# Kernel optimization log

Measured on AMD Instinct MI355X. Metric: run time of the kernel, lower is better.

Reference implementation:

```python
import jax, jax.numpy as jnp
import numpy as np

N, E, K, D = 100000, 3200000, 1024, 11


def setup_inputs() -> dict:
    key = jax.random.key(0)
    ks = jax.random.split(key, 11)
    return {
        "x": jax.random.normal(ks[0], (N, D), jnp.float32),
        "edge_index": jax.random.randint(ks[1], (2, E), 0, N, dtype=jnp.int32),
        "ready_idx": jnp.sort(jax.random.randint(ks[2], (K,), 0, N, dtype=jnp.int32)),
        "W1": jax.random.normal(ks[3], (D, 64), jnp.float32) * 0.2,
        "b1": jax.random.normal(ks[4], (64,), jnp.float32) * 0.02,
        "W2": jax.random.normal(ks[5], (75, 1), jnp.float32) * 0.2,
        "b2": jax.random.normal(ks[6], (1,), jnp.float32) * 0.02,
        "Wd": jax.random.normal(ks[7], (64, 1), jnp.float32) * 0.2,
        "bd": jax.random.normal(ks[8], (1,), jnp.float32) * 0.02,
        "Wv": jax.random.normal(ks[9], (64, 1), jnp.float32) * 0.2,
        "bv": jax.random.normal(ks[10], (1,), jnp.float32) * 0.02,
    }


def gcn_conv(x, W, b, src, dst):
    """PyG GCNConv with flow='target_to_source': gather from dst, aggregate at src.
    Symmetric normalization with self-loops (weight 1)."""
    n = x.shape[0]
    h = x @ W  # [N, F_out]
    loop = jnp.arange(n, dtype=src.dtype)
    s = jnp.concatenate([src, loop])  # aggregation index (row for target_to_source)
    d = jnp.concatenate([dst, loop])  # gather index
    deg = jax.ops.segment_sum(jnp.ones(s.shape, h.dtype), s, num_segments=n)
    dis = jnp.where(deg > 0, jax.lax.rsqrt(jnp.maximum(deg, 1e-12)), 0.0)
    norm = dis[s] * dis[d]  # [E+N]
    out = jax.ops.segment_sum(norm[:, None] * h[d], s, num_segments=n)
    return out + b


def reference(x, edge_index, ready_idx, W1, b1, W2, b2, Wd, bd, Wv, bv):
    src, dst = edge_index[0], edge_index[1]
    h = jax.nn.relu(gcn_conv(x, W1, b1, src, dst))           # [N, 64]
    x_input = jnp.concatenate([h, x], axis=1)                # [N, 75]
    probs_n = gcn_conv(x_input, W2, b2, src, dst)            # [N, 1]
    x_mean = jnp.mean(h, axis=0)                             # [64]
    v = x_mean @ Wv + bv                                     # [1]
    prob_nothing = x_mean @ Wd + bd                          # [1]
    logits = jnp.concatenate([probs_n[ready_idx, 0], prob_nothing])  # [K+1]
    probs = jax.nn.softmax(logits)
    return probs, v
```

## Files before the change

### kernel.cpp

```cpp
#include <hip/hip_runtime.h>
#include <hip/hip_fp16.h>
#include <math.h>

#define N_ 100000
#define E_ 3200000
#define K_ 1024
#define D_ 11
#define NBUCK_ 391
#define NPAD_ (NBUCK_ * 256)
#define CAPB_ 16384
#define CAP_ 32
#define CAPW_ 33
#define GB_ 512
#define CHUNK_ 6256
#define SA_ 8
#define SD_ 4
#define XC_ 32
#define RSEG_ 4096
#define RSTRIDE_ 16

static inline size_t align512(size_t x) { return (x + 511) & ~(size_t)511; }

__device__ inline float2 h2f(unsigned int u) {
    __half2 h = *reinterpret_cast<__half2*>(&u);
    return __half22float2(h);
}

__global__ void k_prep(const float* __restrict__ x, const int* __restrict__ ready,
                       __half* __restrict__ xh,
                       int* __restrict__ deg, float* __restrict__ pr_raw,
                       unsigned char* __restrict__ flag, float* __restrict__ xpart,
                       int* __restrict__ bcur, int* __restrict__ rcntp) {
    int i = blockIdx.x * blockDim.x + threadIdx.x;
    if (i < N_ * 16) {
        int n = i >> 4, j = i & 15;
        if (j < D_) xh[i] = __float2half_rn(x[n * D_ + j]);
    }
    if (i < N_) {
        deg[i] = 0; pr_raw[i] = 0.f;
        int lo = 0, hi = K_ - 1, f = 0;
        while (lo <= hi) {
            int mid = (lo + hi) >> 1;
            int v = ready[mid];
            if (v == i) { f = 1; break; }
            if (v < i) lo = mid + 1; else hi = mid - 1;
        }
        flag[i] = (unsigned char)f;
    }
    if (i < XC_ * 64) xpart[i] = 0.f;
    if (i < NBUCK_) bcur[i] = i * CAPB_;
    if (i < 32 * RSTRIDE_) rcntp[i] = 0;
}

__global__ __launch_bounds__(256) void k_bin(const int* __restrict__ src,
                                             const int* __restrict__ dst,
                                             int* __restrict__ bcur,
                                             int* __restrict__ gbuf) {
    __shared__ int sbuf[NBUCK_ * CAPW_];
    __shared__ int scnt[NBUCK_];
    int t = threadIdx.x;
    for (int b = t; b < NBUCK_; b += 256) scnt[b] = 0;
    __syncthreads();
    long e0 = (long)blockIdx.x * CHUNK_;
    for (int r = 0; r < CHUNK_; r += 2048) {
        int off = r + t * 8;
        long i0 = e0 + off;
        if (off < CHUNK_ && i0 + 7 < E_) {
            int4 s0 = *(const int4*)(src + i0);
            int4 s1 = *(const int4*)(src + i0 + 4);
            int4 d0 = *(const int4*)(dst + i0);
            int4 d1 = *(const int4*)(dst + i0 + 4);
            int ss[8] = {s0.x, s0.y, s0.z, s0.w, s1.x, s1.y, s1.z, s1.w};
            int dd[8] = {d0.x, d0.y, d0.z, d0.w, d1.x, d1.y, d1.z, d1.w};
#pragma unroll
            for (int q = 0; q < 8; q++) {
                int b = ss[q] >> 8;
                int pack = ((ss[q] & 255) << 17) | dd[q];
                int pos = atomicAdd(&scnt[b], 1);
                if (pos < CAP_) sbuf[b * CAPW_ + pos] = pack;
                else gbuf[atomicAdd(&bcur[b], 1)] = pack;
            }
        }
    }
    __syncthreads();
    for (int b = t; b < NBUCK_; b += 256) {
        int c = min(scnt[b], CAP_);
        while (c >= 16) {
            int g = atomicAdd(&bcur[b], 16);
            c -= 16;
            if ((g & 3) == 0) {
                int4* gp = (int4*)(gbuf + g);
#pragma unroll
                for (int q = 0; q < 4; q++)
                    gp[q] = make_int4(sbuf[b*CAPW_ + c + 4*q],
                                      sbuf[b*CAPW_ + c + 4*q + 1],
                                      sbuf[b*CAPW_ + c + 4*q + 2],
                                      sbuf[b*CAPW_ + c + 4*q + 3]);
            } else {
                for (int k = 0; k < 16; k++) gbuf[g + k] = sbuf[b*CAPW_ + c + k];
            }
        }
        if (c > 0) {
            int g = atomicAdd(&bcur[b], c);
            for (int k = 0; k < c; k++) gbuf[g + k] = sbuf[b*CAPW_ + k];
        }
    }
}

__global__ __launch_bounds__(256) void k_deg(const int* __restrict__ bcur,
                                             const int* __restrict__ gbuf,
                                             int* __restrict__ deg) {
    __shared__ int hist[256];
    int t = threadIdx.x, b = blockIdx.x, s = blockIdx.y;
    hist[t] = 0;
    __syncthreads();
    int base = b * CAPB_;
    int cnt = min(bcur[b] - base, CAPB_);
    int seg = (((cnt + SD_ - 1) / SD_) + 3) & ~3;
    int lo = s * seg, hi = min(lo + seg, cnt);
    int p = lo + t * 4;
    for (; p + 3 < hi; p += 1024) {
        int4 v = *(const int4*)(gbuf + base + p);
        atomicAdd(&hist[v.x >> 17], 1);
        atomicAdd(&hist[v.y >> 17], 1);
        atomicAdd(&hist[v.z >> 17], 1);
        atomicAdd(&hist[v.w >> 17], 1);
    }
    if (p < hi) {
        for (int q = p; q < hi; q++) atomicAdd(&hist[gbuf[base + q] >> 17], 1);
    }
    __syncthreads();
    int node = (b << 8) + t;
    if (node < N_ && hist[t]) atomicAdd(&deg[node], hist[t]);
}

__global__ void k_dis(const int* __restrict__ deg, float* __restrict__ dis,
                      __half* __restrict__ xh) {
    int i = blockIdx.x * blockDim.x + threadIdx.x;
    if (i >= N_) return;
    float dv = rsqrtf((float)(deg[i] + 1));
    dis[i] = dv;
    xh[(size_t)i * 16 + 11] = __float2half_rn(dv);
}

__global__ __launch_bounds__(256) void k_agg(const int* __restrict__ bcur,
                                             const int* __restrict__ gbuf,
                                             const __half* __restrict__ xh,
                                             const unsigned char* __restrict__ flag,
                                             float* __restrict__ upart,
                                             int* __restrict__ rcntp,
                                             int2* __restrict__ redge) {
    __shared__ int sorted[2048];
    __shared__ int hist[256];
    __shared__ int incl[256];
    __shared__ int offa[256];
    int t = threadIdx.x, b = blockIdx.x, s = blockIdx.y;
    hist[t] = 0;
    __syncthreads();
    int base = b * CAPB_;
    int cnt = min(bcur[b] - base, CAPB_);
    int seg = (cnt + SA_ - 1) / SA_;
    int lo = s * seg, hi = min(lo + seg, cnt);
    int segn = hi - lo;
    int kmax = (segn + 255) >> 8;
    int pk[8], rk[8];
    for (int k = 0; k < kmax; k++) {
        int idx = lo + (k << 8) + t;
        if (idx < hi) {
            pk[k] = gbuf[base + idx];
            rk[k] = atomicAdd(&hist[pk[k] >> 17], 1);
        } else pk[k] = -1;
    }
    __syncthreads();
    incl[t] = hist[t];
    __syncthreads();
    for (int off = 1; off < 256; off <<= 1) {
        int v = (t >= off) ? incl[t - off] : 0;
        __syncthreads();
        incl[t] += v;
        __syncthreads();
    }
    offa[t] = incl[t] - hist[t];
    __syncthreads();
    for (int k = 0; k < kmax; k++) {
        if (pk[k] >= 0) sorted[offa[pk[k] >> 17] + rk[k]] = pk[k];
    }
    __syncthreads();
    int my_start = offa[t], my_cnt = hist[t];
    int node = (b << 8) + t;
    const uint4* xr = (const uint4*)xh;
    float acc[D_];
#pragma unroll
    for (int j = 0; j < D_; j++) acc[j] = 0.f;
    int i = 0;
    for (; i + 3 < my_cnt; i += 4) {
        int pp[4];
#pragma unroll
        for (int q = 0; q < 4; q++) pp[q] = sorted[my_start + i + q];
        uint4 A[4], B[4];
#pragma unroll
        for (int q = 0; q < 4; q++) {
            size_t r = (size_t)(pp[q] & 131071) * 2;
            A[q] = xr[r]; B[q] = xr[r + 1];
        }
#pragma unroll
        for (int q = 0; q < 4; q++) {
            float2 f0 = h2f(A[q].x), f1 = h2f(A[q].y), f2 = h2f(A[q].z);
            float2 f3 = h2f(A[q].w), f4 = h2f(B[q].x), f5 = h2f(B[q].y);
            float w = f5.y;
            acc[0]  = fmaf(w, f0.x, acc[0]);
            acc[1]  = fmaf(w, f0.y, acc[1]);
            acc[2]  = fmaf(w, f1.x, acc[2]);
            acc[3]  = fmaf(w, f1.y, acc[3]);
            acc[4]  = fmaf(w, f2.x, acc[4]);
            acc[5]  = fmaf(w, f2.y, acc[5]);
            acc[6]  = fmaf(w, f3.x, acc[6]);
            acc[7]  = fmaf(w, f3.y, acc[7]);
            acc[8]  = fmaf(w, f4.x, acc[8]);
            acc[9]  = fmaf(w, f4.y, acc[9]);
            acc[10] = fmaf(w, f5.x, acc[10]);
        }
    }
    for (; i < my_cnt; i++) {
        int pack = sorted[my_start + i];
        size_t r = (size_t)(pack & 131071) * 2;
        uint4 A = xr[r], B = xr[r + 1];
        float2 f0 = h2f(A.x), f1 = h2f(A.y), f2 = h2f(A.z);
        float2 f3 = h2f(A.w), f4 = h2f(B.x), f5 = h2f(B.y);
        float w = f5.y;
        acc[0]  = fmaf(w, f0.x, acc[0]);
        acc[1]  = fmaf(w, f0.y, acc[1]);
        acc[2]  = fmaf(w, f1.x, acc[2]);
        acc[3]  = fmaf(w, f1.y, acc[3]);
        acc[4]  = fmaf(w, f2.x, acc[4]);
        acc[5]  = fmaf(w, f2.y, acc[5]);
        acc[6]  = fmaf(w, f3.x, acc[6]);
        acc[7]  = fmaf(w, f3.y, acc[7]);
        acc[8]  = fmaf(w, f4.x, acc[8]);
        acc[9]  = fmaf(w, f4.y, acc[9]);
        acc[10] = fmaf(w, f5.x, acc[10]);
    }
    float* dst = upart + ((size_t)s * NPAD_ + node) * 12;
    ((float4*)dst)[0] = make_float4(acc[0], acc[1], acc[2],  acc[3]);
    ((float4*)dst)[1] = make_float4(acc[4], acc[5], acc[6],  acc[7]);
    ((float4*)dst)[2] = make_float4(acc[8], acc[9], acc[10], 0.f);

    if (node < N_ && my_cnt > 0 && flag[node]) {
        int r = (b * SA_ + s) & 31;
        int slot = atomicAdd(&rcntp[r * RSTRIDE_], my_cnt);
        int lim = min(my_cnt, max(0, RSEG_ - slot));
        for (int i2 = 0; i2 < lim; i2++)
            redge[(r << 12) + slot + i2] =
                make_int2(node, sorted[my_start + i2] & 131071);
    }
}

__global__ __launch_bounds__(256) void k_node(
    const float* __restrict__ upart, const float* __restrict__ x,
    const float* __restrict__ dis,
    const float* __restrict__ W1, const float* __restrict__ b1,
    const float* __restrict__ W2,
    float* __restrict__ hd, float* __restrict__ xpart) {
    __shared__ float sW1[D_ * 64];
    __shared__ float sb1[64];
    __shared__ float sW2[75];
    __shared__ float smean[64];
    int t = threadIdx.x;
    for (int k = t; k < D_ * 64; k += 256) sW1[k] = W1[k];
    if (t < 64) { sb1[t] = b1[t]; smean[t] = 0.f; }
    if (t < 75) sW2[t] = W2[t];
    __syncthreads();

    int nl = t >> 2, q = t & 3;
    int node = blockIdx.x * 64 + nl;
    bool valid = node < N_;

    float4 mine = make_float4(0.f, 0.f, 0.f, 0.f);
    if (valid && q < 3) {
        const int TOT3 = NPAD_ * 3;
        int slot = node * 3 + q;
        const float4* up = (const float4*)upart;
        float4 a = up[slot];
#pragma unroll
        for (int s = 1; s < SA_; s++) {
            float4 v = up[(size_t)s * TOT3 + slot];
            a.x += v.x; a.y += v.y; a.z += v.z; a.w += v.w;
        }
        mine = a;
    }
    int lb = (t & 63) & ~3;
    float acc[D_];
    acc[0]  = __shfl(mine.x, lb);     acc[1]  = __shfl(mine.y, lb);
    acc[2]  = __shfl(mine.z, lb);     acc[3]  = __shfl(mine.w, lb);
    acc[4]  = __shfl(mine.x, lb + 1); acc[5]  = __shfl(mine.y, lb + 1);
    acc[6]  = __shfl(mine.z, lb + 1); acc[7]  = __shfl(mine.w, lb + 1);
    acc[8]  = __shfl(mine.x, lb + 2); acc[9]  = __shfl(mine.y, lb + 2);
    acc[10] = __shfl(mine.z, lb + 2);

    float hreg[16];
    float h2v = 0.f;
    float di = 0.f;
    if (valid) {
        di = dis[node];
        float xr_[D_], g[D_];
#pragma unroll
        for (int j = 0; j < D_; j++) xr_[j] = x[(size_t)node * D_ + j];
#pragma unroll
        for (int j = 0; j < D_; j++) g[j] = di * (acc[j] + di * xr_[j]);

        int fbase = q << 4;
#pragma unroll
        for (int j = 0; j < 16; j++) {
            int f = fbase + j;
            float a = sb1[f];
#pragma unroll
            for (int jj = 0; jj < D_; jj++) a = fmaf(g[jj], sW1[jj * 64 + f], a);
            float hf = fmaxf(a, 0.f);
            hreg[j] = hf;
            h2v = fmaf(hf, sW2[f], h2v);
        }
        if (q == 0) {
#pragma unroll
            for (int jj = 0; jj < D_; jj++) h2v = fmaf(xr_[jj], sW2[64 + jj], h2v);
        }
    } else {
#pragma unroll
        for (int j = 0; j < 16; j++) hreg[j] = 0.f;
    }
    h2v += __shfl_xor(h2v, 1);
    h2v += __shfl_xor(h2v, 2);
    if (valid && q == 0) hd[node] = di * h2v;

    int lane = t & 63;
#pragma unroll
    for (int j = 0; j < 16; j++) {
        float v = hreg[j];
        v += __shfl_xor(v, 4);
        v += __shfl_xor(v, 8);
        v += __shfl_xor(v, 16);
        v += __shfl_xor(v, 32);
        if (lane < 4) atomicAdd(&smean[(lane << 4) + j], v);
    }
    __syncthreads();
    if (t < 64) atomicAdd(&xpart[((blockIdx.x & (XC_ - 1)) << 6) + t], smean[t]);
}

__global__ void k_pr(const int* __restrict__ rcntp, const int2* __restrict__ redge,
                     const float* __restrict__ hd, float* __restrict__ pr_raw) {
    int idx = blockIdx.x * blockDim.x + threadIdx.x;
    int r = idx >> 12;
    int off = idx & (RSEG_ - 1);
    if (r < 32 && off < min(rcntp[r * RSTRIDE_], RSEG_)) {
        int2 e = redge[(r << 12) + off];
        atomicAdd(&pr_raw[e.x], hd[e.y]);
    }
}

__global__ __launch_bounds__(1024) void k_final(
    const int* __restrict__ ready, const float* __restrict__ dis,
    const float* __restrict__ hd, const float* __restrict__ pr_raw,
    const float* __restrict__ xpart,
    const float* __restrict__ b2,
    const float* __restrict__ Wd, const float* __restrict__ bd,
    const float* __restrict__ Wv, const float* __restrict__ bv,
    float* __restrict__ out) {
    __shared__ float xm[64];
    __shared__ float red[1024];
    __shared__ float s_max, s_sum, s_pn, s_v;
    int t = threadIdx.x;
    if (t < 64) {
        float s = 0.f;
#pragma unroll
        for (int c = 0; c < XC_; c++) s += xpart[(c << 6) + t];
        xm[t] = s * (1.0f / N_);
    }
    __syncthreads();
    if (t == 0) {
        float pn = bd[0], vv = bv[0];
        for (int f = 0; f < 64; f++) { pn += xm[f] * Wd[f]; vv += xm[f] * Wv[f]; }
        s_pn = pn; s_v = vv;
    }
    int r = ready[t];
    float dr = dis[r];
    float l = dr * (pr_raw[r] + hd[r]) + b2[0];
    __syncthreads();
    float pn = s_pn;
    red[t] = (t == 0) ? fmaxf(l, pn) : l;
    __syncthreads();
    for (int sft = 512; sft > 0; sft >>= 1) {
        if (t < sft) red[t] = fmaxf(red[t], red[t + sft]);
        __syncthreads();
    }
    if (t == 0) s_max = red[0];
    __syncthreads();
    float m = s_max;
    float el = expf(l - m);
    red[t] = el + ((t == 0) ? expf(pn - m) : 0.f);
    __syncthreads();
    for (int sft = 512; sft > 0; sft >>= 1) {
        if (t < sft) red[t] += red[t + sft];
        __syncthreads();
    }
    if (t == 0) s_sum = red[0];
    __syncthreads();
    float inv = 1.0f / s_sum;
    out[t] = el * inv;
    if (t == 0) {
        out[K_] = expf(pn - m) * inv;
        out[K_ + 1] = s_v;
    }
}

extern "C" void kernel_launch(void* const* d_in, const int* in_sizes, int n_in,
                              void* d_out, int out_size, void* d_ws, size_t ws_size,
                              hipStream_t stream) {
    const float* x    = (const float*)d_in[0];
    const int*   ei   = (const int*)d_in[1];
    const int*   src  = ei;
    const int*   dst  = ei + E_;
    const int*   ready= (const int*)d_in[2];
    const float* W1   = (const float*)d_in[3];
    const float* b1   = (const float*)d_in[4];
    const float* W2   = (const float*)d_in[5];
    const float* b2   = (const float*)d_in[6];
    const float* Wd   = (const float*)d_in[7];
    const float* bd   = (const float*)d_in[8];
    const float* Wv   = (const float*)d_in[9];
    const float* bv   = (const float*)d_in[10];
    float* out = (float*)d_out;

    char* ws = (char*)d_ws;
    size_t o = 0;
    int*   bcur   = (int*)(ws + o);          o += align512(NBUCK_ * sizeof(int));
    int*   rcntp  = (int*)(ws + o);          o += align512(32 * RSTRIDE_ * sizeof(int));
    int*   gbuf   = (int*)(ws + o);          o += align512((size_t)NBUCK_ * CAPB_ * sizeof(int));
    float* upart  = (float*)(ws + o);        o += align512((size_t)SA_ * NPAD_ * 12 * sizeof(float));
    __half* xh    = (__half*)(ws + o);       o += align512((size_t)N_ * 16 * sizeof(__half));
    int2*  redge  = (int2*)(ws + o);         o += align512((size_t)32 * RSEG_ * sizeof(int2));
    int*   deg    = (int*)(ws + o);          o += align512(N_ * sizeof(int));
    float* dis    = (float*)(ws + o);        o += align512(N_ * sizeof(float));
    float* hd     = (float*)(ws + o);        o += align512(N_ * sizeof(float));
    float* pr_raw = (float*)(ws + o);        o += align512(N_ * sizeof(float));
    unsigned char* flag = (unsigned char*)(ws + o); o += align512(N_);
    float* xpart  = (float*)(ws + o);        o += align512(XC_ * 64 * sizeof(float));

    const int B = 256;
    int g_node  = (N_ + B - 1) / B;
    int g_node4 = (N_ + 63) / 64;
    int g_prep  = (N_ * 16 + B - 1) / B;
    int g_pr    = (32 * RSEG_) / B;
    dim3 gdeg(NBUCK_, SD_);
    dim3 gagg(NBUCK_, SA_);

    k_prep <<<g_prep, B, 0, stream>>>(x, ready, xh, deg, pr_raw, flag, xpart, bcur, rcntp);
    k_bin  <<<GB_, B, 0, stream>>>(src, dst, bcur, gbuf);
    k_deg  <<<gdeg, B, 0, stream>>>(bcur, gbuf, deg);
    k_dis  <<<g_node, B, 0, stream>>>(deg, dis, xh);
    k_agg  <<<gagg, B, 0, stream>>>(bcur, gbuf, xh, flag, upart, rcntp, redge);
    k_node <<<g_node4, B, 0, stream>>>(upart, x, dis, W1, b1, W2, hd, xpart);
    k_pr   <<<g_pr, B, 0, stream>>>(rcntp, redge, hd, pr_raw);
    k_final<<<1, 1024, 0, stream>>>(ready, dis, hd, pr_raw, xpart,
                                    b2, Wd, bd, Wv, bv, out);
}
```

Baseline: 206.5 us.

## Replace per-bucket LDS buffers with block-local counting sort in edge binning

The binning kernel now builds a per-block histogram of source buckets, prefix-scans it, and scatters packed edges into a contiguous shared-memory array sorted by bucket. Each bucket's run is then written to global memory with a single atomic reservation per bucket per block, using four lanes per bucket. This removes the capped per-bucket LDS slots and the per-edge global atomic overflow path. In exchange it adds a 512-entry scan with many barriers and smaller, less coalesced per-bucket global writes, and the chunk size changes from 6256 to 4096 edges per block.

After: 215.2 us. +4.2%, slower.

```diff
diff --git a/kernel.cpp b/kernel.cpp
--- a/kernel.cpp
+++ b/kernel.cpp
@@ -9,10 +9,9 @@
 #define NBUCK_ 391
 #define NPAD_ (NBUCK_ * 256)
 #define CAPB_ 16384
-#define CAP_ 32
-#define CAPW_ 33
-#define GB_ 512
-#define CHUNK_ 6256
+#define GB_ 782
+#define CHUNK_ 4096
+#define KE_ 16
 #define SA_ 8
 #define SD_ 4
 #define XC_ 32
@@ -56,54 +55,71 @@
                                              const int* __restrict__ dst,
                                              int* __restrict__ bcur,
                                              int* __restrict__ gbuf) {
-    __shared__ int sbuf[NBUCK_ * CAPW_];
-    __shared__ int scnt[NBUCK_];
+    __shared__ int hist[NBUCK_ + 1];
+    __shared__ int scan[512];
+    __shared__ int scomp[CHUNK_];
     int t = threadIdx.x;
-    for (int b = t; b < NBUCK_; b += 256) scnt[b] = 0;
-    __syncthreads();
+    for (int b = t; b < NBUCK_ + 1; b += 256) hist[b] = 0;
+    __syncthreads();
+
     long e0 = (long)blockIdx.x * CHUNK_;
-    for (int r = 0; r < CHUNK_; r += 2048) {
-        int off = r + t * 8;
-        long i0 = e0 + off;
-        if (off < CHUNK_ && i0 + 7 < E_) {
+    int pk[KE_];
+    int mt[KE_];
+#pragma unroll
+    for (int r = 0; r < 4; r++) {
+        long i0 = e0 + r * 1024 + t * 4;
+        if (i0 + 3 < E_) {
             int4 s0 = *(const int4*)(src + i0);
-            int4 s1 = *(const int4*)(src + i0 + 4);
             int4 d0 = *(const int4*)(dst + i0);
-            int4 d1 = *(const int4*)(dst + i0 + 4);
-            int ss[8] = {s0.x, s0.y, s0.z, s0.w, s1.x, s1.y, s1.z, s1.w};
-            int dd[8] = {d0.x, d0.y, d0.z, d0.w, d1.x, d1.y, d1.z, d1.w};
-#pragma unroll
-            for (int q = 0; q < 8; q++) {
+            int ss[4] = {s0.x, s0.y, s0.z, s0.w};
+            int dd[4] = {d0.x, d0.y, d0.z, d0.w};
+#pragma unroll
+            for (int q = 0; q < 4; q++) {
                 int b = ss[q] >> 8;
-                int pack = ((ss[q] & 255) << 17) | dd[q];
-                int pos = atomicAdd(&scnt[b], 1);
-                if (pos < CAP_) sbuf[b * CAPW_ + pos] = pack;
-                else gbuf[atomicAdd(&bcur[b], 1)] = pack;
+                pk[r * 4 + q] = ((ss[q] & 255) << 17) | dd[q];
+                int rk = atomicAdd(&hist[b], 1);
+                mt[r * 4 + q] = (b << 13) | rk;
             }
-        }
-    }
-    __syncthreads();
-    for (int b = t; b < NBUCK_; b += 256) {
-        int c = min(scnt[b], CAP_);
-        while (c >= 16) {
-            int g = atomicAdd(&bcur[b], 16);
-            c -= 16;
-            if ((g & 3) == 0) {
-                int4* gp = (int4*)(gbuf + g);
-#pragma unroll
-                for (int q = 0; q < 4; q++)
-                    gp[q] = make_int4(sbuf[b*CAPW_ + c + 4*q],
-                                      sbuf[b*CAPW_ + c + 4*q + 1],
-                                      sbuf[b*CAPW_ + c + 4*q + 2],
-                                      sbuf[b*CAPW_ + c + 4*q + 3]);
-            } else {
-                for (int k = 0; k < 16; k++) gbuf[g + k] = sbuf[b*CAPW_ + c + k];
-            }
-        }
-        if (c > 0) {
-            int g = atomicAdd(&bcur[b], c);
-            for (int k = 0; k < c; k++) gbuf[g + k] = sbuf[b*CAPW_ + k];
-        }
+        } else {
+#pragma unroll
+            for (int q = 0; q < 4; q++) pk[r * 4 + q] = -1;
+        }
+    }
+    __syncthreads();
+
+    scan[t] = hist[t];
+    scan[256 + t] = (256 + t < NBUCK_) ? hist[256 + t] : 0;
+    __syncthreads();
+    for (int off = 1; off < 512; off <<= 1) {
+        int v0 = (t >= off) ? scan[t - off] : 0;
+        int v1 = scan[256 + t - off];
+        __syncthreads();
+        scan[t] += v0;
+        scan[256 + t] += v1;
+        __syncthreads();
+    }
+
+#pragma unroll
+    for (int k = 0; k < KE_; k++) {
+        if (pk[k] != -1) {
+            int b = mt[k] >> 13, rk = mt[k] & 8191;
+            scomp[scan[b] - hist[b] + rk] = pk[k];
+        }
+    }
+    __syncthreads();
+
+    int lane = t & 63;
+    int qid = t >> 2;
+    int ql = t & 3;
+    for (int b = qid; b < NBUCK_; b += 64) {
+        int c = hist[b];
+        if (c == 0) continue;
+        int off = scan[b] - c;
+        int g = 0;
+        if (ql == 0) g = atomicAdd(&bcur[b], c);
+        g = __shfl(g, lane & ~3);
+        for (int k = ql; k < c; k += 4)
+            gbuf[g + k] = scomp[off + k];
     }
 }
 
```
